# Performance work log

Measured on AMD Instinct MI355X. Metric: run time of the kernel, lower is better.

Reference implementation:

```python
import jax, jax.numpy as jnp
import numpy as np
import math

N = 50000      # nodes
E = 800000     # edges (avg degree 16)
T = 4          # time steps
F = 64         # feature dim (in = hidden = out)
MAX_LEN = 200  # positional encoding table length
EPS = 1e-5     # BatchNorm eps


def _make_pe(time_dim, max_len):
    pe = np.zeros((max_len, time_dim), dtype=np.float32)
    position = np.arange(max_len, dtype=np.float32)[:, None]
    div_term = np.exp(np.arange(0, time_dim, 2, dtype=np.float32) * (-math.log(10000.0) / time_dim))
    pe[:, 0::2] = np.sin(position * div_term)
    pe[:, 1::2] = np.cos(position * div_term)
    return jnp.asarray(pe)


def setup_inputs() -> dict:
    key = jax.random.key(0)
    ks = jax.random.split(key, 10)
    xav = math.sqrt(2.0 / (F + F))  # xavier_normal_ std for square linear
    return {
        "node_features": jax.random.normal(ks[0], (N, T, F), dtype=jnp.float32),
        "edges_weight": jax.random.uniform(ks[1], (T, E), dtype=jnp.float32),
        "identities": jax.random.randint(ks[2], (T,), 0, MAX_LEN),
        "edge_src": jax.random.randint(ks[3], (E,), 0, N),
        "edge_dst": jax.random.randint(ks[4], (E,), 0, N),
        "pe": _make_pe(F, MAX_LEN),
        "W0": jax.random.normal(ks[5], (F, F), dtype=jnp.float32) * xav,
        "W1": jax.random.normal(ks[6], (F, F), dtype=jnp.float32) * xav,
        "g0": jnp.ones((F,), jnp.float32),
        "b0": jnp.zeros((F,), jnp.float32),
        "g1": jnp.ones((F,), jnp.float32),
        "b1": jnp.zeros((F,), jnp.float32),
    }


def _gcn_layer(h, ew, edge_src, edge_dst, W):
    # gather-mul-scatter: msg_e = h[src_e] * w_e ; agg_v = sum_{e: dst=v} msg_e
    msg = h[edge_src] * ew                                   # (E, T, F)
    agg = jax.ops.segment_sum(msg, edge_dst, num_segments=N)  # (N, T, F)
    readout = agg.mean(axis=0)                                # dgl.mean_nodes (single graph) -> (T, F)
    return agg @ W, readout @ W


def _batchnorm(x, gamma, beta):
    # training-mode batch stats over all non-channel dims
    mean = x.mean(axis=(0, 1))
    var = x.var(axis=(0, 1))
    return (x - mean) * jax.lax.rsqrt(var + EPS) * gamma + beta


def reference(node_features, edges_weight, identities, edge_src, edge_dst,
              pe, W0, W1, g0, b0, g1, b1):
    # positional encoding added per time step
    h = node_features + pe[identities]          # (N, T, F)
    ew = edges_weight.T[:, :, None]             # (E, T, 1)
    # layer 0: gcn -> dropout(eval=identity) -> BN -> ReLU
    h, readout = _gcn_layer(h, ew, edge_src, edge_dst, W0)
    h = jax.nn.relu(_batchnorm(h, g0, b0))
    # layer 1 (output layer)
    h, readout = _gcn_layer(h, ew, edge_src, edge_dst, W1)
    h = jax.nn.relu(_batchnorm(h, g1, b1))
    return h, readout
```

## Files before the change

kernel.cpp:

```cpp
#include <hip/hip_runtime.h>

#define TF 256

typedef __attribute__((ext_vector_type(8))) short short8;
typedef __attribute__((ext_vector_type(4))) float f32x4;
typedef __attribute__((ext_vector_type(4))) unsigned int uint4v;
typedef __attribute__((ext_vector_type(2))) unsigned int uint2v;

__device__ inline unsigned short f2bf(float x) {
  unsigned u = __float_as_uint(x);
  u += 0x7fffu + ((u >> 16) & 1u);
  return (unsigned short)(u >> 16);
}
__device__ inline unsigned pack2(unsigned short lo, unsigned short hi) {
  return (unsigned)lo | ((unsigned)hi << 16);
}
__device__ inline float bflo(unsigned u) { return __uint_as_float(u << 16); }
__device__ inline float bfhi(unsigned u) { return __uint_as_float(u & 0xffff0000u); }

__global__ void prep_kernel(const float* __restrict__ x, const float* __restrict__ pe,
                            const int* __restrict__ ids, uint2v* __restrict__ h0, int n4,
                            const float* __restrict__ W0, const float* __restrict__ W1,
                            short* __restrict__ wf0, short* __restrict__ wf1) {
  const int tid = threadIdx.x;
  const int gid = blockIdx.x * blockDim.x + tid;
  const int stride = gridDim.x * blockDim.x;
  for (int i = gid; i < n4; i += stride) {
    int e0 = (i << 2) & (TF - 1);
    int t = e0 >> 6;
    int f4 = e0 & 63;
    f32x4 v = __builtin_nontemporal_load(&reinterpret_cast<const f32x4*>(x)[i]);
    const f32x4 p = *reinterpret_cast<const f32x4*>(&pe[ids[t] * 64 + f4]);
    uint2v o;
    o.x = pack2(f2bf(v.x + p.x), f2bf(v.y + p.y));
    o.y = pack2(f2bf(v.z + p.z), f2bf(v.w + p.w));
    h0[i] = o;
  }
  if (blockIdx.x == gridDim.x - 1) {
    const int lane = tid & 63;
    #pragma unroll
    for (int fi = 0; fi < 2; ++fi) {
      const int frag = (tid >> 6) + fi * 4;
      const int c = frag >> 1, h = frag & 1;
      const int col = (c << 4) + (lane & 15);
      const int k0 = h * 32 + ((lane >> 4) << 3);
      short* o0 = wf0 + frag * 512 + lane * 8;
      short* o1 = wf1 + frag * 512 + lane * 8;
      #pragma unroll
      for (int i = 0; i < 8; ++i) {
        o0[i] = (short)f2bf(W0[(k0 + i) * 64 + col]);
        o1[i] = (short)f2bf(W1[(k0 + i) * 64 + col]);
      }
    }
  }
}

__global__ __launch_bounds__(256) void binscatter_kernel(
    const int* __restrict__ src, const int* __restrict__ dst,
    const float* __restrict__ ew, int* __restrict__ gbin_cursor,
    uint4v* __restrict__ tmp, int E, int nbins) {
  __shared__ int hist[256];
  __shared__ int hist2[256];
  __shared__ int basearr[256];
  const int tid = threadIdx.x;
  hist[tid] = 0;
  hist2[tid] = 0;
  __syncthreads();
  const int epb = (E + gridDim.x - 1) / gridDim.x;
  const int beg = blockIdx.x * epb;
  const int end = min(beg + epb, E);
  for (int e = beg + tid; e < end; e += 256)
    atomicAdd(&hist[__builtin_nontemporal_load(&dst[e]) >> 8], 1);
  __syncthreads();
  if (tid < nbins && hist[tid] > 0)
    basearr[tid] = atomicAdd(&gbin_cursor[tid], hist[tid]);
  __syncthreads();
  for (int e = beg + tid; e < end; e += 256) {
    const int d = dst[e];
    const int bin = d >> 8;
    const int idx = atomicAdd(&hist2[bin], 1);
    uint4v ent;
    ent.x = (unsigned)(src[e] << 9);
    ent.y = pack2(f2bf(ew[e]), f2bf(ew[(size_t)E + e]));
    ent.z = pack2(f2bf(ew[2 * (size_t)E + e]), f2bf(ew[3 * (size_t)E + e]));
    ent.w = (unsigned)d;
    const int pos = basearr[bin] + idx;
    if (pos < 8192)
      tmp[((size_t)bin << 13) + pos] = ent;
  }
}

__global__ __launch_bounds__(256) void csr_build_kernel(
    const uint4v* __restrict__ tmp, const int* __restrict__ gbin_counts,
    int* __restrict__ offsets, uint4v* __restrict__ csr_ent, int n, int nbins) {
  __shared__ int hist[256];
  __shared__ int lbase[256];
  __shared__ int wsum[4];
  __shared__ int binbase_s;
  const int bin = blockIdx.x;
  const int tid = threadIdx.x;
  const int lane = tid & 63;
  const int wid = tid >> 6;
  hist[tid] = 0;

  int c = (tid < bin) ? gbin_counts[tid] : 0;
  int s = c;
  #pragma unroll
  for (int o = 1; o < 64; o <<= 1) s += __shfl_xor(s, o, 64);
  if (lane == 0) wsum[wid] = s;
  __syncthreads();
  if (tid == 0) binbase_s = wsum[0] + wsum[1] + wsum[2] + wsum[3];
  __syncthreads();
  const int binbase = binbase_s;

  const int cnt = min(gbin_counts[bin], 8192);
  const uint4v* bt = tmp + ((size_t)bin << 13);

  for (int i = tid; i < cnt; i += 256)
    atomicAdd(&hist[(int)(bt[i].w & 255u)], 1);
  __syncthreads();

  int v = hist[tid];
  int sc = v;
  #pragma unroll
  for (int o = 1; o < 64; o <<= 1) {
    int t = __shfl_up(sc, o, 64);
    if (lane >= o) sc += t;
  }
  if (lane == 63) wsum[wid] = sc;
  __syncthreads();
  if (tid == 0) {
    int acc = 0;
    #pragma unroll
    for (int w = 0; w < 4; ++w) { int t = wsum[w]; wsum[w] = acc; acc += t; }
  }
  __syncthreads();
  const int excl = sc - v + wsum[wid] + binbase;
  lbase[tid] = excl;
  const int node = (bin << 8) + tid;
  if (node < n) offsets[node] = excl;
  if (node == n - 1) offsets[n] = binbase + cnt;
  __syncthreads();

  for (int i = tid; i < cnt; i += 256) {
    uint4v ent = bt[i];
    const int local = (int)(ent.w & 255u);
    const int pos = atomicAdd(&lbase[local], 1);
    ent.w = 0u;
    csr_ent[pos] = ent;
  }
}

template <int LAYER>
__global__ __launch_bounds__(256, 6) void fused_agg_mm_kernel(
    const char* __restrict__ h_base, const int* __restrict__ offsets,
    const uint4v* __restrict__ csr_ent, const short* __restrict__ wf,
    const float* __restrict__ red, const float* __restrict__ g,
    const float* __restrict__ b, float inv_count,
    unsigned short* __restrict__ y_bf, float* __restrict__ part, int n_groups) {
  __shared__ unsigned short tile[2][16][72];
  __shared__ float s_sc[64], s_sh[64];
  const int tid = threadIdx.x;
  const int lane = tid & 63;
  const int wid = tid >> 6;
  if (LAYER == 1) {
    if (tid < 64) {
      float sum = red[tid] + red[64 + tid] + red[128 + tid] + red[192 + tid];
      float mean = sum * inv_count;
      float var = red[256 + tid] * inv_count - mean * mean;
      float sc = g[tid] * rsqrtf(var + 1e-5f);
      s_sc[tid] = sc;
      s_sh[tid] = fmaf(-mean, sc, b[tid]);
    }
    __syncthreads();
  }
  const short8 bf0 = *reinterpret_cast<const short8*>(wf + (wid * 2 + 0) * 512 + lane * 8);
  const short8 bf1 = *reinterpret_cast<const short8*>(wf + (wid * 2 + 1) * 512 + lane * 8);

  const int p = lane >> 5;
  const unsigned q = lane & 31;
  const unsigned qb = q << 4;
  const int tw = q >> 3;

  float scv[8], shv[8];
  if (LAYER == 1) {
    const int f0 = (q & 7) << 3;
    #pragma unroll
    for (int j = 0; j < 8; ++j) { scv[j] = s_sc[f0 + j]; shv[j] = s_sh[f0 + j]; }
  }

  f32x4 csum = (f32x4){0.f, 0.f, 0.f, 0.f};
  float ssq = 0.f;
  int buf = 0;

  for (int grp = blockIdx.x; grp < n_groups; grp += gridDim.x) {
    const int v = grp * 4 + wid;
    float acc[8];
    #pragma unroll
    for (int j = 0; j < 8; ++j) acc[j] = 0.f;

    auto wext = [&](uint4v ent) -> float {
      unsigned word = (tw & 2) ? ent.z : ent.y;
      return (tw & 1) ? bfhi(word) : bflo(word);
    };
    auto body = [&](uint4v u, float w) {
      float x[8] = {bflo(u.x), bfhi(u.x), bflo(u.y), bfhi(u.y),
                    bflo(u.z), bfhi(u.z), bflo(u.w), bfhi(u.w)};
      #pragma unroll
      for (int j = 0; j < 8; ++j) {
        float t = x[j];
        if (LAYER == 1) t = fmaxf(0.f, fmaf(t, scv[j], shv[j]));
        acc[j] = fmaf(w, t, acc[j]);
      }
    };

    const int beg = offsets[v];
    const int end = offsets[v + 1];
    int i = beg;
    for (; i + 8 <= end; i += 8) {
      uint4v ent[4];
      #pragma unroll
      for (int c = 0; c < 4; ++c) ent[c] = csr_ent[i + 2 * c + p];
      uint4v row[4];
      #pragma unroll
      for (int c = 0; c < 4; ++c)
        row[c] = *reinterpret_cast<const uint4v*>(h_base + (ent[c].x + qb));
      #pragma unroll
      for (int c = 0; c < 4; ++c) body(row[c], wext(ent[c]));
    }
    for (; i + 2 <= end; i += 2) {
      const uint4v ent = csr_ent[i + p];
      const uint4v row = *reinterpret_cast<const uint4v*>(h_base + (ent.x + qb));
      body(row, wext(ent));
    }
    if (i < end) {
      const uint4v ent = csr_ent[i];
      const uint4v row = *reinterpret_cast<const uint4v*>(h_base + (ent.x + qb));
      body(row, p == 0 ? wext(ent) : 0.f);
    }

    #pragma unroll
    for (int j = 0; j < 8; ++j) acc[j] += __shfl_xor(acc[j], 32, 64);
    if (lane < 32) {
      uint4v o;
      o.x = pack2(f2bf(acc[0]), f2bf(acc[1]));
      o.y = pack2(f2bf(acc[2]), f2bf(acc[3]));
      o.z = pack2(f2bf(acc[4]), f2bf(acc[5]));
      o.w = pack2(f2bf(acc[6]), f2bf(acc[7]));
      *reinterpret_cast<uint4v*>(&tile[buf][wid * 4 + (q >> 3)][(q & 7) * 8]) = o;
    }
    __syncthreads();

    const int r = lane & 15;
    const int k0 = (lane >> 4) << 3;
    const short8 a0 = *reinterpret_cast<const short8*>(&tile[buf][r][k0]);
    const short8 a1 = *reinterpret_cast<const short8*>(&tile[buf][r][k0 + 32]);
    f32x4 dacc = (f32x4){0.f, 0.f, 0.f, 0.f};
    dacc = __builtin_amdgcn_mfma_f32_16x16x32_bf16(a0, bf0, dacc, 0, 0, 0);
    dacc = __builtin_amdgcn_mfma_f32_16x16x32_bf16(a1, bf1, dacc, 0, 0, 0);
    const int gbase = grp * 16 + ((lane >> 4) << 2);
    const int col = (wid << 4) + (lane & 15);
    #pragma unroll
    for (int i2 = 0; i2 < 4; ++i2) {
      const float val = dacc[i2];
      y_bf[(size_t)(gbase + i2) * 64 + col] = f2bf(val);
      csum[i2] += val;
      ssq += val * val;
    }
    buf ^= 1;
  }

  #pragma unroll
  for (int i2 = 0; i2 < 4; ++i2) {
    float vv = csum[i2];
    vv += __shfl_xor(vv, 16, 64);
    vv += __shfl_xor(vv, 32, 64);
    csum[i2] = vv;
  }
  float qq = ssq;
  qq += __shfl_xor(qq, 16, 64);
  qq += __shfl_xor(qq, 32, 64);
  if (lane < 16) {
    #pragma unroll
    for (int i2 = 0; i2 < 4; ++i2)
      part[(size_t)blockIdx.x * 320 + i2 * 64 + (wid << 4) + lane] = csum[i2];
    part[(size_t)blockIdx.x * 320 + 256 + (wid << 4) + lane] = qq;
  }
}

__global__ __launch_bounds__(1024) void reduce_part_kernel(const float* __restrict__ part,
                                                           float* __restrict__ red, int nblk) {
  __shared__ float lds[1024];
  const int tid = threadIdx.x;
  const int col = blockIdx.x * 16 + (tid & 15);
  const int r = tid >> 4;
  float s = 0.f;
  for (int bk = r; bk < nblk; bk += 64) s += part[(size_t)bk * 320 + col];
  lds[tid] = s;
  __syncthreads();
  #pragma unroll
  for (int off = 512; off >= 16; off >>= 1) {
    if (tid < off) lds[tid] += lds[tid + off];
    __syncthreads();
  }
  if (tid < 16) red[col] = lds[tid];
}

__global__ __launch_bounds__(256) void bn_relu_out_kernel(
    const uint4v* __restrict__ yb, const float* __restrict__ red,
    const float* __restrict__ g, const float* __restrict__ b, float inv_count,
    float* __restrict__ out_readout, float invN, f32x4* __restrict__ out, int n8) {
  __shared__ float s_sc[64], s_sh[64];
  const int tid = threadIdx.x;
  if (tid < 64) {
    float sum = red[tid] + red[64 + tid] + red[128 + tid] + red[192 + tid];
    float mean = sum * inv_count;
    float var = red[256 + tid] * inv_count - mean * mean;
    float sc = g[tid] * rsqrtf(var + 1e-5f);
    s_sc[tid] = sc;
    s_sh[tid] = fmaf(-mean, sc, b[tid]);
  }
  __syncthreads();
  if (blockIdx.x == 0) out_readout[tid] = red[tid] * invN;
  const int i = blockIdx.x * 256 + tid;
  if (i >= n8) return;
  const int f0 = (i & 7) << 3;
  uint4v u = __builtin_nontemporal_load(&yb[i]);
  float x[8] = {bflo(u.x), bfhi(u.x), bflo(u.y), bfhi(u.y),
                bflo(u.z), bfhi(u.z), bflo(u.w), bfhi(u.w)};
  f32x4 o0, o1;
  o0.x = fmaxf(0.f, fmaf(x[0], s_sc[f0 + 0], s_sh[f0 + 0]));
  o0.y = fmaxf(0.f, fmaf(x[1], s_sc[f0 + 1], s_sh[f0 + 1]));
  o0.z = fmaxf(0.f, fmaf(x[2], s_sc[f0 + 2], s_sh[f0 + 2]));
  o0.w = fmaxf(0.f, fmaf(x[3], s_sc[f0 + 3], s_sh[f0 + 3]));
  o1.x = fmaxf(0.f, fmaf(x[4], s_sc[f0 + 4], s_sh[f0 + 4]));
  o1.y = fmaxf(0.f, fmaf(x[5], s_sc[f0 + 5], s_sh[f0 + 5]));
  o1.z = fmaxf(0.f, fmaf(x[6], s_sc[f0 + 6], s_sh[f0 + 6]));
  o1.w = fmaxf(0.f, fmaf(x[7], s_sc[f0 + 7], s_sh[f0 + 7]));
  __builtin_nontemporal_store(o0, &out[i * 2 + 0]);
  __builtin_nontemporal_store(o1, &out[i * 2 + 1]);
}

extern "C" void kernel_launch(void* const* d_in, const int* in_sizes, int n_in,
                              void* d_out, int out_size, void* d_ws, size_t ws_size,
                              hipStream_t stream) {
  const float* node_features = (const float*)d_in[0];
  const float* edges_weight  = (const float*)d_in[1];
  const int*   identities    = (const int*)d_in[2];
  const int*   edge_src      = (const int*)d_in[3];
  const int*   edge_dst      = (const int*)d_in[4];
  const float* pe            = (const float*)d_in[5];
  const float* W0            = (const float*)d_in[6];
  const float* W1            = (const float*)d_in[7];
  const float* g0            = (const float*)d_in[8];
  const float* b0            = (const float*)d_in[9];
  const float* g1            = (const float*)d_in[10];
  const float* b1            = (const float*)d_in[11];

  const int T = in_sizes[2];
  const int E = in_sizes[3];
  const int F = in_sizes[8];
  const int N = in_sizes[0] / (T * F);
  const int R = N * T;
  const int nbins = (N + 255) >> 8;

  float* out = (float*)d_out;
  float* out_h = out;
  float* out_readout = out + (size_t)N * T * F;

  char* ws = (char*)d_ws;
  size_t off = 0;
  auto alloc = [&](size_t bytes) -> void* {
    off = (off + 255) & ~(size_t)255;
    void* p = ws + off;
    off += bytes;
    return p;
  };
  int*    gbin_cursor = (int*)alloc(256 * sizeof(int));
  int*    offsets  = (int*)alloc(((size_t)N + 1) * sizeof(int));
  uint4v* csr_ent  = (uint4v*)alloc(((size_t)E + 16) * 16);
  uint4v* tmp      = (uint4v*)alloc(((size_t)nbins << 13) * 16);
  unsigned short* h0b  = (unsigned short*)alloc((size_t)N * TF * 2);
  unsigned short* y0b  = (unsigned short*)alloc((size_t)N * TF * 2);
  short* wf0 = (short*)alloc(8 * 512 * sizeof(short));
  short* wf1 = (short*)alloc(8 * 512 * sizeof(short));
  const int FB = 1536;
  float* mm_part = (float*)alloc((size_t)FB * 320 * sizeof(float));
  float* red     = (float*)alloc(320 * sizeof(float));
  (void)ws_size;

  const float invR = 1.0f / (float)R;
  const int n_groups = N / 4;

  (void)hipMemsetAsync(gbin_cursor, 0, 256 * sizeof(int), stream);
  hipLaunchKernelGGL(binscatter_kernel, dim3(512), dim3(256), 0, stream,
                     edge_src, edge_dst, edges_weight, gbin_cursor, tmp, E, nbins);
  hipLaunchKernelGGL(csr_build_kernel, dim3(nbins), dim3(256), 0, stream,
                     tmp, gbin_cursor, offsets, csr_ent, N, nbins);
  hipLaunchKernelGGL(prep_kernel, dim3(2048), dim3(256), 0, stream,
                     node_features, pe, identities, (uint2v*)h0b, (N * TF) / 4,
                     W0, W1, wf0, wf1);

  hipLaunchKernelGGL((fused_agg_mm_kernel<0>), dim3(FB), dim3(256), 0, stream,
                     (const char*)h0b, offsets, csr_ent, wf0,
                     nullptr, nullptr, nullptr, 0.f, y0b, mm_part, n_groups);
  hipLaunchKernelGGL(reduce_part_kernel, dim3(20), dim3(1024), 0, stream, mm_part, red, FB);

  hipLaunchKernelGGL((fused_agg_mm_kernel<1>), dim3(FB), dim3(256), 0, stream,
                     (const char*)y0b, offsets, csr_ent, wf1,
                     red, g0, b0, invR, h0b , mm_part, n_groups);
  hipLaunchKernelGGL(reduce_part_kernel, dim3(20), dim3(1024), 0, stream, mm_part, red, FB);

  hipLaunchKernelGGL(bn_relu_out_kernel, dim3((R * 8 + 255) / 256), dim3(256), 0, stream,
                     (const uint4v*)h0b, red, g1, b1, invR,
                     out_readout, 1.0f / (float)N, (f32x4*)out_h, R * 8);
}
```

Baseline: 231.4 us.

## Group nodes by in-degree via permutation to balance wavefront work in aggregation

Builds a degree histogram during CSR construction, scans it, and scatters node ids into a permutation sorted by (clamped) in-degree. The fused aggregation+matmul kernels then process nodes in this order, so the four wavefronts in a block handle similar-degree nodes and the MFMA tile waits less on the slowest one. Output rows are written back to each node's original position. This adds two small kernels and an extra perm load per group, and it breaks the contiguous row locality of the output writes.

```diff
diff --git a/kernel.cpp b/kernel.cpp
--- a/kernel.cpp
+++ b/kernel.cpp
@@ -92,7 +92,8 @@
 
 __global__ __launch_bounds__(256) void csr_build_kernel(
     const uint4v* __restrict__ tmp, const int* __restrict__ gbin_counts,
-    int* __restrict__ offsets, uint4v* __restrict__ csr_ent, int n, int nbins) {
+    int* __restrict__ offsets, uint4v* __restrict__ csr_ent,
+    int* __restrict__ gdeghist, int n, int nbins) {
   __shared__ int hist[256];
   __shared__ int lbase[256];
   __shared__ int wsum[4];
@@ -121,6 +122,8 @@
   __syncthreads();
 
   int v = hist[tid];
+  const int node = (bin << 8) + tid;
+  if (node < n) atomicAdd(&gdeghist[min(v, 63)], 1);
   int sc = v;
   #pragma unroll
   for (int o = 1; o < 64; o <<= 1) {
@@ -137,7 +140,6 @@
   __syncthreads();
   const int excl = sc - v + wsum[wid] + binbase;
   lbase[tid] = excl;
-  const int node = (bin << 8) + tid;
   if (node < n) offsets[node] = excl;
   if (node == n - 1) offsets[n] = binbase + cnt;
   __syncthreads();
@@ -151,10 +153,34 @@
   }
 }
 
+__global__ __launch_bounds__(64) void perm_scan_kernel(const int* __restrict__ gdeghist,
+                                                       int* __restrict__ dbase) {
+  const int i = threadIdx.x;
+  int v = gdeghist[i];
+  int s = v;
+  #pragma unroll
+  for (int o = 1; o < 64; o <<= 1) {
+    int t = __shfl_up(s, o, 64);
+    if (i >= o) s += t;
+  }
+  dbase[i] = s - v;
+}
+
+__global__ void perm_scatter_kernel(const int* __restrict__ offsets, int* __restrict__ dbase,
+                                    int* __restrict__ perm, int n) {
+  const int i = blockIdx.x * blockDim.x + threadIdx.x;
+  if (i >= n) return;
+  int deg = offsets[i + 1] - offsets[i];
+  deg = min(deg, 63);
+  const int pos = atomicAdd(&dbase[deg], 1);
+  perm[pos] = i;
+}
+
 template <int LAYER>
 __global__ __launch_bounds__(256, 6) void fused_agg_mm_kernel(
     const char* __restrict__ h_base, const int* __restrict__ offsets,
     const uint4v* __restrict__ csr_ent, const short* __restrict__ wf,
+    const int* __restrict__ perm,
     const float* __restrict__ red, const float* __restrict__ g,
     const float* __restrict__ b, float inv_count,
     unsigned short* __restrict__ y_bf, float* __restrict__ part, int n_groups) {
@@ -194,7 +220,8 @@
   int buf = 0;
 
   for (int grp = blockIdx.x; grp < n_groups; grp += gridDim.x) {
-    const int v = grp * 4 + wid;
+    const int v = perm[(grp << 2) + wid];
+    const int pv = perm[(grp << 2) + (lane >> 4)];
     float acc[8];
     #pragma unroll
     for (int j = 0; j < 8; ++j) acc[j] = 0.f;
@@ -258,12 +285,11 @@
     f32x4 dacc = (f32x4){0.f, 0.f, 0.f, 0.f};
     dacc = __builtin_amdgcn_mfma_f32_16x16x32_bf16(a0, bf0, dacc, 0, 0, 0);
     dacc = __builtin_amdgcn_mfma_f32_16x16x32_bf16(a1, bf1, dacc, 0, 0, 0);
-    const int gbase = grp * 16 + ((lane >> 4) << 2);
     const int col = (wid << 4) + (lane & 15);
     #pragma unroll
     for (int i2 = 0; i2 < 4; ++i2) {
       const float val = dacc[i2];
-      y_bf[(size_t)(gbase + i2) * 64 + col] = f2bf(val);
+      y_bf[(size_t)(pv * 4 + i2) * 64 + col] = f2bf(val);
       csum[i2] += val;
       ssq += val * val;
     }
@@ -287,6 +313,7 @@
     part[(size_t)blockIdx.x * 320 + 256 + (wid << 4) + lane] = qq;
   }
 }
+
 
 __global__ __launch_bounds__(1024) void reduce_part_kernel(const float* __restrict__ part,
                                                            float* __restrict__ red, int nblk) {
@@ -376,8 +403,12 @@
     off += bytes;
     return p;
   };
-  int*    gbin_cursor = (int*)alloc(256 * sizeof(int));
+  int* zeros = (int*)alloc(384 * sizeof(int));
+  int* gbin_cursor = zeros;
+  int* gdeghist    = zeros + 256;
+  int* dbase       = zeros + 320;
   int*    offsets  = (int*)alloc(((size_t)N + 1) * sizeof(int));
+  int*    perm     = (int*)alloc((size_t)N * sizeof(int));
   uint4v* csr_ent  = (uint4v*)alloc(((size_t)E + 16) * 16);
   uint4v* tmp      = (uint4v*)alloc(((size_t)nbins << 13) * 16);
   unsigned short* h0b  = (unsigned short*)alloc((size_t)N * TF * 2);
@@ -392,22 +423,25 @@
   const float invR = 1.0f / (float)R;
   const int n_groups = N / 4;
 
-  (void)hipMemsetAsync(gbin_cursor, 0, 256 * sizeof(int), stream);
+  (void)hipMemsetAsync(zeros, 0, 384 * sizeof(int), stream);
   hipLaunchKernelGGL(binscatter_kernel, dim3(512), dim3(256), 0, stream,
                      edge_src, edge_dst, edges_weight, gbin_cursor, tmp, E, nbins);
   hipLaunchKernelGGL(csr_build_kernel, dim3(nbins), dim3(256), 0, stream,
-                     tmp, gbin_cursor, offsets, csr_ent, N, nbins);
+                     tmp, gbin_cursor, offsets, csr_ent, gdeghist, N, nbins);
+  hipLaunchKernelGGL(perm_scan_kernel, dim3(1), dim3(64), 0, stream, gdeghist, dbase);
+  hipLaunchKernelGGL(perm_scatter_kernel, dim3((N + 255) / 256), dim3(256), 0, stream,
+                     offsets, dbase, perm, N);
   hipLaunchKernelGGL(prep_kernel, dim3(2048), dim3(256), 0, stream,
                      node_features, pe, identities, (uint2v*)h0b, (N * TF) / 4,
                      W0, W1, wf0, wf1);
 
   hipLaunchKernelGGL((fused_agg_mm_kernel<0>), dim3(FB), dim3(256), 0, stream,
-                     (const char*)h0b, offsets, csr_ent, wf0,
+                     (const char*)h0b, offsets, csr_ent, wf0, perm,
                      nullptr, nullptr, nullptr, 0.f, y0b, mm_part, n_groups);
   hipLaunchKernelGGL(reduce_part_kernel, dim3(20), dim3(1024), 0, stream, mm_part, red, FB);
 
   hipLaunchKernelGGL((fused_agg_mm_kernel<1>), dim3(FB), dim3(256), 0, stream,
-                     (const char*)y0b, offsets, csr_ent, wf1,
+                     (const char*)y0b, offsets, csr_ent, wf1, perm,
                      red, g0, b0, invR, h0b , mm_part, n_groups);
   hipLaunchKernelGGL(reduce_part_kernel, dim3(20), dim3(1024), 0, stream, mm_part, red, FB);
 
```

Result: slower. 489.4 us (+111.5%).

## Reorder nodes by degree within bins to balance wavefront work in aggregation

Applied to the files above, without the earlier changes.

The CSR build now counting-sorts the nodes in each 256-node bin by in-degree and writes a permutation array. Both aggregation kernels take node ids from this permutation, so the four wavefronts of a block handle nodes of similar degree and wait less for one another at the block barrier. Output rows are written to the permuted node's location. The cost is an extra indirection per group and scattered output stores; the sort is local to a bin, so locality within the bin is kept.

```diff
diff --git a/kernel.cpp b/kernel.cpp
--- a/kernel.cpp
+++ b/kernel.cpp
@@ -92,16 +92,20 @@
 
 __global__ __launch_bounds__(256) void csr_build_kernel(
     const uint4v* __restrict__ tmp, const int* __restrict__ gbin_counts,
-    int* __restrict__ offsets, uint4v* __restrict__ csr_ent, int n, int nbins) {
+    int* __restrict__ offsets, uint4v* __restrict__ csr_ent,
+    int* __restrict__ perm, int n, int nbins) {
   __shared__ int hist[256];
   __shared__ int lbase[256];
   __shared__ int wsum[4];
   __shared__ int binbase_s;
+  __shared__ int deghist[64];
+  __shared__ int degbase[64];
   const int bin = blockIdx.x;
   const int tid = threadIdx.x;
   const int lane = tid & 63;
   const int wid = tid >> 6;
   hist[tid] = 0;
+  if (tid < 64) deghist[tid] = 0;
 
   int c = (tid < bin) ? gbin_counts[tid] : 0;
   int s = c;
@@ -121,6 +125,9 @@
   __syncthreads();
 
   int v = hist[tid];
+  const int node = (bin << 8) + tid;
+  const int degc = min(v, 63);
+  if (node < n) atomicAdd(&deghist[degc], 1);
   int sc = v;
   #pragma unroll
   for (int o = 1; o < 64; o <<= 1) {
@@ -137,10 +144,25 @@
   __syncthreads();
   const int excl = sc - v + wsum[wid] + binbase;
   lbase[tid] = excl;
-  const int node = (bin << 8) + tid;
   if (node < n) offsets[node] = excl;
   if (node == n - 1) offsets[n] = binbase + cnt;
   __syncthreads();
+
+  if (tid < 64) {
+    int dv = deghist[tid];
+    int ds = dv;
+    #pragma unroll
+    for (int o = 1; o < 64; o <<= 1) {
+      int t = __shfl_up(ds, o, 64);
+      if (tid >= o) ds += t;
+    }
+    degbase[tid] = ds - dv;
+  }
+  __syncthreads();
+  if (node < n) {
+    const int rank = atomicAdd(&degbase[degc], 1);
+    perm[(bin << 8) + rank] = node;
+  }
 
   for (int i = tid; i < cnt; i += 256) {
     uint4v ent = bt[i];
@@ -155,6 +177,7 @@
 __global__ __launch_bounds__(256, 6) void fused_agg_mm_kernel(
     const char* __restrict__ h_base, const int* __restrict__ offsets,
     const uint4v* __restrict__ csr_ent, const short* __restrict__ wf,
+    const int* __restrict__ perm,
     const float* __restrict__ red, const float* __restrict__ g,
     const float* __restrict__ b, float inv_count,
     unsigned short* __restrict__ y_bf, float* __restrict__ part, int n_groups) {
@@ -194,7 +217,8 @@
   int buf = 0;
 
   for (int grp = blockIdx.x; grp < n_groups; grp += gridDim.x) {
-    const int v = grp * 4 + wid;
+    const int v = perm[(grp << 2) + wid];
+    const int pv = perm[(grp << 2) + (lane >> 4)];
     float acc[8];
     #pragma unroll
     for (int j = 0; j < 8; ++j) acc[j] = 0.f;
@@ -258,12 +282,11 @@
     f32x4 dacc = (f32x4){0.f, 0.f, 0.f, 0.f};
     dacc = __builtin_amdgcn_mfma_f32_16x16x32_bf16(a0, bf0, dacc, 0, 0, 0);
     dacc = __builtin_amdgcn_mfma_f32_16x16x32_bf16(a1, bf1, dacc, 0, 0, 0);
-    const int gbase = grp * 16 + ((lane >> 4) << 2);
     const int col = (wid << 4) + (lane & 15);
     #pragma unroll
     for (int i2 = 0; i2 < 4; ++i2) {
       const float val = dacc[i2];
-      y_bf[(size_t)(gbase + i2) * 64 + col] = f2bf(val);
+      y_bf[(size_t)(pv * 4 + i2) * 64 + col] = f2bf(val);
       csum[i2] += val;
       ssq += val * val;
     }
@@ -378,6 +401,7 @@
   };
   int*    gbin_cursor = (int*)alloc(256 * sizeof(int));
   int*    offsets  = (int*)alloc(((size_t)N + 1) * sizeof(int));
+  int*    perm     = (int*)alloc((size_t)N * sizeof(int));
   uint4v* csr_ent  = (uint4v*)alloc(((size_t)E + 16) * 16);
   uint4v* tmp      = (uint4v*)alloc(((size_t)nbins << 13) * 16);
   unsigned short* h0b  = (unsigned short*)alloc((size_t)N * TF * 2);
@@ -396,18 +420,18 @@
   hipLaunchKernelGGL(binscatter_kernel, dim3(512), dim3(256), 0, stream,
                      edge_src, edge_dst, edges_weight, gbin_cursor, tmp, E, nbins);
   hipLaunchKernelGGL(csr_build_kernel, dim3(nbins), dim3(256), 0, stream,
-                     tmp, gbin_cursor, offsets, csr_ent, N, nbins);
+                     tmp, gbin_cursor, offsets, csr_ent, perm, N, nbins);
   hipLaunchKernelGGL(prep_kernel, dim3(2048), dim3(256), 0, stream,
                      node_features, pe, identities, (uint2v*)h0b, (N * TF) / 4,
                      W0, W1, wf0, wf1);
 
   hipLaunchKernelGGL((fused_agg_mm_kernel<0>), dim3(FB), dim3(256), 0, stream,
-                     (const char*)h0b, offsets, csr_ent, wf0,
+                     (const char*)h0b, offsets, csr_ent, wf0, perm,
                      nullptr, nullptr, nullptr, 0.f, y0b, mm_part, n_groups);
   hipLaunchKernelGGL(reduce_part_kernel, dim3(20), dim3(1024), 0, stream, mm_part, red, FB);
 
   hipLaunchKernelGGL((fused_agg_mm_kernel<1>), dim3(FB), dim3(256), 0, stream,
-                     (const char*)y0b, offsets, csr_ent, wf1,
+                     (const char*)y0b, offsets, csr_ent, wf1, perm,
                      red, g0, b0, invR, h0b , mm_part, n_groups);
   hipLaunchKernelGGL(reduce_part_kernel, dim3(20), dim3(1024), 0, stream, mm_part, red, FB);
 
```

New measurement: 255.5 us. +10.4%, slower.
